# Kernel tuning notes

Hardware: AMD Instinct MI355X
Metric: run time of the kernel (lower is better)

Reference implementation:

```python
import jax, jax.numpy as jnp
import numpy as np

N_NODES = 50000
N_EDGES = 800000
D_IN = 256
D_OUT = 256


def setup_inputs() -> dict:
    key = jax.random.key(0)
    ks = jax.random.split(key, 8)
    x = jax.random.normal(ks[0], (N_NODES, D_IN), dtype=jnp.float32)
    edge_index = jax.random.randint(ks[1], (2, N_EDGES), 0, N_NODES, dtype=jnp.int64)
    W_src = jax.random.normal(ks[2], (D_IN, D_OUT), dtype=jnp.float32) * 0.05
    b_src = jax.random.normal(ks[3], (D_OUT,), dtype=jnp.float32) * 0.05
    W_dst = jax.random.normal(ks[4], (D_IN, D_OUT), dtype=jnp.float32) * 0.05
    b_dst = jax.random.normal(ks[5], (D_OUT,), dtype=jnp.float32) * 0.05
    W_self = jax.random.normal(ks[6], (D_IN, D_OUT), dtype=jnp.float32) * 0.05
    b_self = jax.random.normal(ks[7], (D_OUT,), dtype=jnp.float32) * 0.05
    return {"x": x, "edge_index": edge_index, "W_src": W_src, "b_src": b_src,
            "W_dst": W_dst, "b_dst": b_dst, "W_self": W_self, "b_self": b_self}


def reference(x, edge_index, W_src, b_src, W_dst, b_dst, W_self, b_self):
    # LEConv: messages = src_linear(x[row]) - dst_linear(x[col]);
    # scatter-add messages into destination nodes (col); add self_linear(x).
    # Linear commutes with row-gather, so project once on [N, d] then gather.
    row, col = edge_index[0], edge_index[1]
    src = x @ W_src + b_src            # [N, D_OUT]
    dst = x @ W_dst + b_dst            # [N, D_OUT]
    messages = src[row] - dst[col]     # [E, D_OUT]
    agg = jax.ops.segment_sum(messages, col, num_segments=x.shape[0])  # [N, D_OUT]
    return x @ W_self + b_self + agg
```

## Files before the change

kernel.cpp:

```cpp
#include <hip/hip_runtime.h>

#define D 256

typedef unsigned short ushort_t;
typedef unsigned int uint_t;
typedef __attribute__((ext_vector_type(8))) short short8;
typedef __attribute__((ext_vector_type(4))) float floatx4;

static __device__ __forceinline__ ushort_t f2bf(float f) {
    union { float f; uint_t u; } c; c.f = f;
    uint_t r = (c.u + 0x7FFFu + ((c.u >> 16) & 1u)) >> 16;
    return (ushort_t)r;
}
static __device__ __forceinline__ float bf2f(ushort_t b) {
    union { uint_t u; float f; } c; c.u = ((uint_t)b) << 16;
    return c.f;
}

static __device__ __forceinline__ void async16(const void* g, void* l) {
    __builtin_amdgcn_global_load_lds(
        (const __attribute__((address_space(1))) void*)g,
        (__attribute__((address_space(3))) void*)l, 16, 0, 0);
}

__global__ void prep_kernel(const int* __restrict__ col, int* __restrict__ deg,
                            int* __restrict__ rank,
                            const float* __restrict__ x, ushort_t* __restrict__ xh,
                            const float* __restrict__ Wself, const float* __restrict__ Wsrc,
                            const float* __restrict__ Wdst, ushort_t* __restrict__ BT,
                            int E, int total8, int degB, int cvtB) {
    int b = blockIdx.x;
    if (b < degB) {
        int e = b * 256 + threadIdx.x;
        if (e < E) rank[e] = atomicAdd(&deg[col[e]], 1);
    } else if (b < degB + cvtB) {
        int i = (b - degB) * 256 + threadIdx.x;
        if (i >= total8) return;
        float4 a = ((const float4*)x)[i * 2];
        float4 bb = ((const float4*)x)[i * 2 + 1];
        uint4 o;
        o.x = f2bf(a.x) | ((uint_t)f2bf(a.y) << 16);
        o.y = f2bf(a.z) | ((uint_t)f2bf(a.w) << 16);
        o.z = f2bf(bb.x) | ((uint_t)f2bf(bb.y) << 16);
        o.w = f2bf(bb.z) | ((uint_t)f2bf(bb.w) << 16);
        ((uint4*)xh)[i] = o;
    } else {
        int id = (b - degB - cvtB) * 256 + threadIdx.x;
        if (id >= 256 * 768) return;
        int j = id / 768, k = id % 768;
        float v;
        if (k < 256)      v = Wself[(size_t)k * 256 + j];
        else if (k < 512) v = Wsrc [(size_t)(k - 256) * 256 + j];
        else              v = Wdst [(size_t)(k - 512) * 256 + j];
        BT[id] = f2bf(v);
    }
}

__global__ __launch_bounds__(256) void scanA(const int* __restrict__ deg,
                                             int* __restrict__ off,
                                             int* __restrict__ partials, int n4) {
    __shared__ int wtot[4];
    const int tid = threadIdx.x, lane = tid & 63, wid = tid >> 6;
    int i4 = blockIdx.x * 256 + tid;
    int4 v = (i4 < n4) ? ((const int4*)deg)[i4] : make_int4(0, 0, 0, 0);
    int s = v.x + v.y + v.z + v.w;
    int incl = s;
    #pragma unroll
    for (int st = 1; st < 64; st <<= 1) {
        int t = __shfl_up(incl, st, 64);
        if (lane >= st) incl += t;
    }
    if (lane == 63) wtot[wid] = incl;
    __syncthreads();
    int wbase = 0;
    #pragma unroll
    for (int w = 0; w < 4; ++w) if (w < wid) wbase += wtot[w];
    int excl = incl - s + wbase;
    if (i4 < n4) {
        int4 o;
        o.x = excl; o.y = o.x + v.x; o.z = o.y + v.y; o.w = o.z + v.z;
        ((int4*)off)[i4] = o;
    }
    if (tid == 0) partials[blockIdx.x] = wtot[0] + wtot[1] + wtot[2] + wtot[3];
}

__global__ __launch_bounds__(256) void scanC(int* __restrict__ off,
                                             const int* __restrict__ partials, int n4) {
    __shared__ int base_s;
    const int tid = threadIdx.x;
    if (tid < 64) {
        int v = (tid < blockIdx.x) ? partials[tid] : 0;
        #pragma unroll
        for (int st = 32; st; st >>= 1) v += __shfl_down(v, st, 64);
        if (tid == 0) base_s = v;
    }
    __syncthreads();
    int base = base_s;
    int i4 = blockIdx.x * 256 + tid;
    if (i4 < n4) {
        int4 o = ((int4*)off)[i4];
        o.x += base; o.y += base; o.z += base; o.w += base;
        ((int4*)off)[i4] = o;
    }
}

__global__ void fill_kernel(const int* __restrict__ row, const int* __restrict__ col,
                            const int* __restrict__ rank, const int* __restrict__ off,
                            int* __restrict__ bucket, int E) {
    int e = blockIdx.x * blockDim.x + threadIdx.x;
    if (e >= E) return;
    bucket[off[col[e]] + rank[e]] = row[e];
}

__global__ __launch_bounds__(256) void segsum_kernel(const ushort_t* __restrict__ xh,
                                                     const int* __restrict__ off,
                                                     const int* __restrict__ deg,
                                                     const int* __restrict__ bucket,
                                                     ushort_t* __restrict__ Gh, int N) {
    int node = blockIdx.x * 4 + (threadIdx.x >> 6);
    int lane = threadIdx.x & 63;
    if (node >= N) return;
    int start = off[node];
    int cnt = deg[node];
    float a0 = 0.f, a1 = 0.f, a2 = 0.f, a3 = 0.f;
    int i = 0;
    for (; i + 4 <= cnt; i += 4) {
        int r0 = bucket[start + i];
        int r1 = bucket[start + i + 1];
        int r2 = bucket[start + i + 2];
        int r3 = bucket[start + i + 3];
        ushort4 v0 = ((const ushort4*)(xh + (size_t)r0 * D))[lane];
        ushort4 v1 = ((const ushort4*)(xh + (size_t)r1 * D))[lane];
        ushort4 v2 = ((const ushort4*)(xh + (size_t)r2 * D))[lane];
        ushort4 v3 = ((const ushort4*)(xh + (size_t)r3 * D))[lane];
        a0 += (bf2f(v0.x) + bf2f(v1.x)) + (bf2f(v2.x) + bf2f(v3.x));
        a1 += (bf2f(v0.y) + bf2f(v1.y)) + (bf2f(v2.y) + bf2f(v3.y));
        a2 += (bf2f(v0.z) + bf2f(v1.z)) + (bf2f(v2.z) + bf2f(v3.z));
        a3 += (bf2f(v0.w) + bf2f(v1.w)) + (bf2f(v2.w) + bf2f(v3.w));
    }
    for (; i < cnt; ++i) {
        int r0 = bucket[start + i];
        ushort4 v0 = ((const ushort4*)(xh + (size_t)r0 * D))[lane];
        a0 += bf2f(v0.x); a1 += bf2f(v0.y); a2 += bf2f(v0.z); a3 += bf2f(v0.w);
    }
    ushort4 o;
    o.x = f2bf(a0); o.y = f2bf(a1); o.z = f2bf(a2); o.w = f2bf(a3);
    ((ushort4*)(Gh + (size_t)node * D))[lane] = o;
}

__global__ __launch_bounds__(256, 4) void mfma_gemm(
    const ushort_t* __restrict__ xh, const ushort_t* __restrict__ Gh,
    const ushort_t* __restrict__ BT, const int* __restrict__ deg,
    const float* __restrict__ bsrc, const float* __restrict__ bdst,
    const float* __restrict__ bself, float* __restrict__ out, int N)
{
    __shared__ ushort_t As[2][4][64][8];
    __shared__ ushort_t Bs[2][8][64][8];

    const int tid = threadIdx.x;
    const int lane = tid & 63, wave = tid >> 6;
    const int quad = lane >> 4, l15 = lane & 15;
    const int wr = wave >> 1, wc = wave & 1;
    const int mbase = blockIdx.x * 64, nbase = blockIdx.y * 128;

    int ar = mbase + wave * 16 + l15; if (ar >= N) ar = N - 1;
    const size_t aoff = (size_t)ar * 256 + quad * 8;
    const ushort_t* bp0 = BT + (size_t)(nbase + (wave * 2) * 16 + l15) * 768 + quad * 8;
    const ushort_t* bp1 = BT + (size_t)(nbase + (wave * 2 + 1) * 16 + l15) * 768 + quad * 8;

    float negdeg[2];
    #pragma unroll
    for (int im = 0; im < 2; ++im) {
        int r = mbase + (wr * 2 + im) * 16 + l15; if (r >= N) r = N - 1;
        negdeg[im] = -(float)deg[r];
    }

    floatx4 acc[2][4] = {};

    async16(xh + aoff, &As[0][wave][0][0]);
    async16(bp0, &Bs[0][wave * 2][0][0]);
    async16(bp1, &Bs[0][wave * 2 + 1][0][0]);
    asm volatile("s_waitcnt vmcnt(0)" ::: "memory");
    __builtin_amdgcn_s_barrier();

    #pragma unroll
    for (int kt = 0; kt < 24; ++kt) {
        const int cur = kt & 1, nxt = cur ^ 1;

        if (kt < 23) {
            const int k1 = kt + 1;
            const ushort_t* Ap = (k1 < 8) ? xh : (k1 < 16 ? Gh : xh);
            const int ka = (k1 & 7) * 32;
            async16(Ap + aoff + ka, &As[nxt][wave][0][0]);
            async16(bp0 + k1 * 32, &Bs[nxt][wave * 2][0][0]);
            async16(bp1 + k1 * 32, &Bs[nxt][wave * 2 + 1][0][0]);
        }

        short8 af[2], bfr[4];
        #pragma unroll
        for (int im = 0; im < 2; ++im)
            af[im] = *(const short8*)(&As[cur][wr * 2 + im][lane][0]);
        #pragma unroll
        for (int in = 0; in < 4; ++in)
            bfr[in] = *(const short8*)(&Bs[cur][wc * 4 + in][lane][0]);
        asm volatile("s_waitcnt lgkmcnt(0)" ::: "memory");

        if (kt >= 16) {
            #pragma unroll
            for (int im = 0; im < 2; ++im) {
                short8 t = af[im];
                #pragma unroll
                for (int j = 0; j < 8; ++j) {
                    float f = bf2f((ushort_t)t[j]) * negdeg[im];
                    t[j] = (short)f2bf(f);
                }
                af[im] = t;
            }
        }

        #pragma unroll
        for (int im = 0; im < 2; ++im)
            #pragma unroll
            for (int in = 0; in < 4; ++in)
                acc[im][in] = __builtin_amdgcn_mfma_f32_16x16x32_bf16(
                    af[im], bfr[in], acc[im][in], 0, 0, 0);

        if (kt < 23) {
            asm volatile("s_waitcnt vmcnt(0)" ::: "memory");
            __builtin_amdgcn_s_barrier();
        }
    }

    float degv[2][4];
    #pragma unroll
    for (int im = 0; im < 2; ++im)
        #pragma unroll
        for (int r = 0; r < 4; ++r) {
            int gm = mbase + wr * 32 + im * 16 + quad * 4 + r;
            degv[im][r] = (gm < N) ? (float)deg[gm] : 0.f;
        }

    #pragma unroll
    for (int in = 0; in < 4; ++in) {
        int gn = nbase + wc * 64 + in * 16 + l15;
        float bs = bself[gn];
        float db = bsrc[gn] - bdst[gn];
        #pragma unroll
        for (int im = 0; im < 2; ++im) {
            #pragma unroll
            for (int r = 0; r < 4; ++r) {
                int gm = mbase + wr * 32 + im * 16 + quad * 4 + r;
                if (gm < N) {
                    out[(size_t)gm * 256 + gn] =
                        acc[im][in][r] + bs + degv[im][r] * db;
                }
            }
        }
    }
}

extern "C" void kernel_launch(void* const* d_in, const int* in_sizes, int n_in,
                              void* d_out, int out_size, void* d_ws, size_t ws_size,
                              hipStream_t stream) {
    const float* x     = (const float*)d_in[0];
    const int*   eidx  = (const int*)d_in[1];
    const float* Wsrc  = (const float*)d_in[2];
    const float* bsrc  = (const float*)d_in[3];
    const float* Wdst  = (const float*)d_in[4];
    const float* bdst  = (const float*)d_in[5];
    const float* Wself = (const float*)d_in[6];
    const float* bself = (const float*)d_in[7];
    float* out = (float*)d_out;

    const int N = in_sizes[0] / D;
    const int E = in_sizes[1] / 2;
    const int* row = eidx;
    const int* col = eidx + E;

    char* p = (char*)d_ws;
    ushort_t* xh  = (ushort_t*)p;        p += (size_t)N * D * sizeof(ushort_t);
    ushort_t* Gh  = (ushort_t*)p;        int* rank = (int*)p;
                                         p += (size_t)N * D * sizeof(ushort_t);
    ushort_t* BT  = (ushort_t*)p;        p += (size_t)768 * 256 * sizeof(ushort_t);
    int* deg      = (int*)p;             p += (size_t)N * sizeof(int);
    int* off      = (int*)p;             p += (size_t)N * sizeof(int);
    int* partials = (int*)p;             p += 64 * sizeof(int);
    int* bucket   = (int*)p;

    hipMemsetAsync(deg, 0, (size_t)N * sizeof(int), stream);

    const int total8 = N * D / 8;
    const int degB = (E + 255) / 256;
    const int cvtB = (total8 + 255) / 256;
    const int btB  = (256 * 768 + 255) / 256;
    prep_kernel<<<degB + cvtB + btB, 256, 0, stream>>>(col, deg, rank, x, xh,
                                                       Wself, Wsrc, Wdst, BT,
                                                       E, total8, degB, cvtB);
    const int n4 = N / 4;
    const int nblk = (n4 + 255) / 256;
    scanA<<<nblk, 256, 0, stream>>>(deg, off, partials, n4);
    scanC<<<nblk, 256, 0, stream>>>(off, partials, n4);
    fill_kernel<<<(E + 255) / 256, 256, 0, stream>>>(row, col, rank, off, bucket, E);
    segsum_kernel<<<(N + 3) / 4, 256, 0, stream>>>(xh, off, deg, bucket, Gh, N);

    dim3 grid((N + 63) / 64, 2);
    mfma_gemm<<<grid, 256, 0, stream>>>(xh, Gh, BT, deg, bsrc, bdst, bself, out, N);
}
```

Baseline: 300.9 us.

## Restructure MFMA GEMM to 128x256 tiles reusing x fragments across two weight blocks

The GEMM now has each block compute a 128-row by full 256-column tile. A fragments are loaded straight from global memory into registers, and each x fragment is reused for both the self/src and the negated-degree dst weight blocks. This cuts the K loop from 24 to 16 steps and removes the duplicate read of x for the dst term. It also drops the A-tile LDS staging and uses partial vmcnt waits to keep loads in flight. The cost is a larger accumulator register footprint and occupancy lowered to 2 blocks per CU, with uncoalesced direct global A loads.

```diff
diff --git a/kernel.cpp b/kernel.cpp
--- a/kernel.cpp
+++ b/kernel.cpp
@@ -148,111 +148,133 @@
     ((ushort4*)(Gh + (size_t)node * D))[lane] = o;
 }
 
-__global__ __launch_bounds__(256, 4) void mfma_gemm(
+__global__ __launch_bounds__(256, 2) void mfma_gemm(
     const ushort_t* __restrict__ xh, const ushort_t* __restrict__ Gh,
     const ushort_t* __restrict__ BT, const int* __restrict__ deg,
     const float* __restrict__ bsrc, const float* __restrict__ bdst,
     const float* __restrict__ bself, float* __restrict__ out, int N)
 {
-    __shared__ ushort_t As[2][4][64][8];
-    __shared__ ushort_t Bs[2][8][64][8];
+    __shared__ ushort_t Bs[2][16][64][8];
+    __shared__ ushort_t Bd[2][16][64][8];
 
     const int tid = threadIdx.x;
     const int lane = tid & 63, wave = tid >> 6;
     const int quad = lane >> 4, l15 = lane & 15;
     const int wr = wave >> 1, wc = wave & 1;
-    const int mbase = blockIdx.x * 64, nbase = blockIdx.y * 128;
-
-    int ar = mbase + wave * 16 + l15; if (ar >= N) ar = N - 1;
-    const size_t aoff = (size_t)ar * 256 + quad * 8;
-    const ushort_t* bp0 = BT + (size_t)(nbase + (wave * 2) * 16 + l15) * 768 + quad * 8;
-    const ushort_t* bp1 = BT + (size_t)(nbase + (wave * 2 + 1) * 16 + l15) * 768 + quad * 8;
-
-    float negdeg[2];
-    #pragma unroll
-    for (int im = 0; im < 2; ++im) {
-        int r = mbase + (wr * 2 + im) * 16 + l15; if (r >= N) r = N - 1;
+    const int mbase = blockIdx.x * 128;
+
+    size_t aoff[4];
+    float negdeg[4];
+    #pragma unroll
+    for (int im = 0; im < 4; ++im) {
+        int r = mbase + wr * 64 + im * 16 + l15;
+        if (r >= N) r = N - 1;
+        aoff[im] = (size_t)r * 256 + (size_t)(quad * 8);
         negdeg[im] = -(float)deg[r];
     }
 
-    floatx4 acc[2][4] = {};
-
-    async16(xh + aoff, &As[0][wave][0][0]);
-    async16(bp0, &Bs[0][wave * 2][0][0]);
-    async16(bp1, &Bs[0][wave * 2 + 1][0][0]);
-    asm volatile("s_waitcnt vmcnt(0)" ::: "memory");
-    __builtin_amdgcn_s_barrier();
-
-    #pragma unroll
-    for (int kt = 0; kt < 24; ++kt) {
-        const int cur = kt & 1, nxt = cur ^ 1;
-
-        if (kt < 23) {
-            const int k1 = kt + 1;
-            const ushort_t* Ap = (k1 < 8) ? xh : (k1 < 16 ? Gh : xh);
-            const int ka = (k1 & 7) * 32;
-            async16(Ap + aoff + ka, &As[nxt][wave][0][0]);
-            async16(bp0 + k1 * 32, &Bs[nxt][wave * 2][0][0]);
-            async16(bp1 + k1 * 32, &Bs[nxt][wave * 2 + 1][0][0]);
-        }
-
-        short8 af[2], bfr[4];
-        #pragma unroll
-        for (int im = 0; im < 2; ++im)
-            af[im] = *(const short8*)(&As[cur][wr * 2 + im][lane][0]);
-        #pragma unroll
-        for (int in = 0; in < 4; ++in)
-            bfr[in] = *(const short8*)(&Bs[cur][wc * 4 + in][lane][0]);
-        asm volatile("s_waitcnt lgkmcnt(0)" ::: "memory");
-
-        if (kt >= 16) {
-            #pragma unroll
-            for (int im = 0; im < 2; ++im) {
-                short8 t = af[im];
+    const ushort_t* bpg[4];
+    #pragma unroll
+    for (int t = 0; t < 4; ++t)
+        bpg[t] = BT + (size_t)((wave * 4 + t) * 16 + l15) * 768 + quad * 8;
+
+    floatx4 acc[4][8] = {};
+    short8 af[2][4];
+
+    auto issueB = [&](int s) {
+        const int b = s & 1;
+        if (s < 8) {
+            const int kb = s * 32;
+            #pragma unroll
+            for (int t = 0; t < 4; ++t)
+                async16(bpg[t] + kb, &Bs[b][wave * 4 + t][0][0]);
+            #pragma unroll
+            for (int t = 0; t < 4; ++t)
+                async16(bpg[t] + 512 + kb, &Bd[b][wave * 4 + t][0][0]);
+        } else {
+            const int kb = 256 + (s - 8) * 32;
+            #pragma unroll
+            for (int t = 0; t < 4; ++t)
+                async16(bpg[t] + kb, &Bs[b][wave * 4 + t][0][0]);
+        }
+    };
+    auto loadA = [&](int s) {
+        const ushort_t* Ap = (s < 8) ? xh : Gh;
+        const int ka = (s & 7) * 32;
+        #pragma unroll
+        for (int im = 0; im < 4; ++im)
+            af[s & 1][im] = *(const short8*)(Ap + aoff[im] + ka);
+    };
+
+    issueB(0);
+    loadA(0);
+
+    #pragma unroll
+    for (int s = 0; s < 16; ++s) {
+        const int cur = s & 1;
+
+        if (s < 15) { issueB(s + 1); loadA(s + 1); }
+
+        if (s < 7)        asm volatile("s_waitcnt vmcnt(12)" ::: "memory");
+        else if (s < 15)  asm volatile("s_waitcnt vmcnt(8)"  ::: "memory");
+        else              asm volatile("s_waitcnt vmcnt(0)"  ::: "memory");
+        __builtin_amdgcn_s_barrier();
+
+        #pragma unroll
+        for (int jn = 0; jn < 8; ++jn) {
+            short8 bf = *(const short8*)(&Bs[cur][wc * 8 + jn][lane][0]);
+            #pragma unroll
+            for (int im = 0; im < 4; ++im)
+                acc[im][jn] = __builtin_amdgcn_mfma_f32_16x16x32_bf16(
+                    af[cur][im], bf, acc[im][jn], 0, 0, 0);
+        }
+        if (s < 8) {
+            short8 afd[4];
+            #pragma unroll
+            for (int im = 0; im < 4; ++im) {
+                short8 t = af[cur][im];
                 #pragma unroll
                 for (int j = 0; j < 8; ++j) {
                     float f = bf2f((ushort_t)t[j]) * negdeg[im];
                     t[j] = (short)f2bf(f);
                 }
-                af[im] = t;
+                afd[im] = t;
             }
-        }
-
-        #pragma unroll
-        for (int im = 0; im < 2; ++im)
-            #pragma unroll
-            for (int in = 0; in < 4; ++in)
-                acc[im][in] = __builtin_amdgcn_mfma_f32_16x16x32_bf16(
-                    af[im], bfr[in], acc[im][in], 0, 0, 0);
-
-        if (kt < 23) {
-            asm volatile("s_waitcnt vmcnt(0)" ::: "memory");
-            __builtin_amdgcn_s_barrier();
-        }
-    }
-
-    float degv[2][4];
-    #pragma unroll
-    for (int im = 0; im < 2; ++im)
+            #pragma unroll
+            for (int jn = 0; jn < 8; ++jn) {
+                short8 bf = *(const short8*)(&Bd[cur][wc * 8 + jn][lane][0]);
+                #pragma unroll
+                for (int im = 0; im < 4; ++im)
+                    acc[im][jn] = __builtin_amdgcn_mfma_f32_16x16x32_bf16(
+                        afd[im], bf, acc[im][jn], 0, 0, 0);
+            }
+        }
+
+        if (s < 15) __builtin_amdgcn_s_barrier();
+    }
+
+    float degv[4][4];
+    #pragma unroll
+    for (int im = 0; im < 4; ++im)
         #pragma unroll
         for (int r = 0; r < 4; ++r) {
-            int gm = mbase + wr * 32 + im * 16 + quad * 4 + r;
+            int gm = mbase + wr * 64 + im * 16 + quad * 4 + r;
             degv[im][r] = (gm < N) ? (float)deg[gm] : 0.f;
         }
 
     #pragma unroll
-    for (int in = 0; in < 4; ++in) {
-        int gn = nbase + wc * 64 + in * 16 + l15;
+    for (int jn = 0; jn < 8; ++jn) {
+        int gn = wc * 128 + jn * 16 + l15;
         float bs = bself[gn];
         float db = bsrc[gn] - bdst[gn];
         #pragma unroll
-        for (int im = 0; im < 2; ++im) {
+        for (int im = 0; im < 4; ++im) {
             #pragma unroll
             for (int r = 0; r < 4; ++r) {
-                int gm = mbase + wr * 32 + im * 16 + quad * 4 + r;
+                int gm = mbase + wr * 64 + im * 16 + quad * 4 + r;
                 if (gm < N) {
                     out[(size_t)gm * 256 + gn] =
-                        acc[im][in][r] + bs + degv[im][r] * db;
+                        acc[im][jn][r] + bs + degv[im][r] * db;
                 }
             }
         }
@@ -303,6 +325,6 @@
     fill_kernel<<<(E + 255) / 256, 256, 0, stream>>>(row, col, rank, off, bucket, E);
     segsum_kernel<<<(N + 3) / 4, 256, 0, stream>>>(xh, off, deg, bucket, Gh, N);
 
-    dim3 grid((N + 63) / 64, 2);
-    mfma_gemm<<<grid, 256, 0, stream>>>(xh, Gh, BT, deg, bsrc, bdst, bself, out, N);
-}
+    mfma_gemm<<<(N + 127) / 128, 256, 0, stream>>>(xh, Gh, BT, deg,
+                                                   bsrc, bdst, bself, out, N);
+}
```

After: 279.2 us. 1.08x faster.
